# Optimization experiments

Hardware: AMD Instinct MI355X
Metric: run time of the kernel (lower is better)

## Reference

```python
import jax, jax.numpy as jnp
import numpy as np

NUM_HEADS = 8

def _proj(x, w, b):
    # 1x1x1 Conv3d == pointwise linear over channel dim
    return jnp.einsum('bcxyz,oc->boxyz', x, w) + b[None, :, None, None, None]


def setup_inputs() -> dict:
    key = jax.random.key(0)
    ks = jax.random.split(key, 9)
    B, C, X, Y, Z = 2, 256, 48, 48, 48
    s = 0.05
    return {
        'x':  jax.random.normal(ks[0], (B, C, X, Y, Z), dtype=jnp.float32),
        'wq': jax.random.normal(ks[1], (C, C), dtype=jnp.float32) * s,
        'bq': jax.random.normal(ks[2], (C,), dtype=jnp.float32) * s,
        'wk': jax.random.normal(ks[3], (C, C), dtype=jnp.float32) * s,
        'bk': jax.random.normal(ks[4], (C,), dtype=jnp.float32) * s,
        'wv': jax.random.normal(ks[5], (C, C), dtype=jnp.float32) * s,
        'bv': jax.random.normal(ks[6], (C,), dtype=jnp.float32) * s,
        'wo': jax.random.normal(ks[7], (C, C), dtype=jnp.float32) * s,
        'bo': jax.random.normal(ks[8], (C,), dtype=jnp.float32) * s,
    }


def reference(x, wq, bq, wk, bk, wv, bv, wo, bo):
    B, C, X, Y, Z = x.shape
    H = NUM_HEADS
    P = C // H  # per-head channels
    q = _proj(x, wq, bq).reshape(B, H, P, X, Y, Z)
    k = _proj(x, wk, bk).reshape(B, H, P, X, Y, Z)
    v = _proj(x, wv, bv).reshape(B, H, P, X, Y, Z)
    # torch einsum 'bnxyzc,bmxyzc->bnmxy' contracts z and per-head channel c
    scores = jnp.einsum('bncxyz,bmcxyz->bnmxy', q, k) / jnp.sqrt(jnp.float32(P))
    # torch F.softmax(dim=-1) on [b,n,m,x,y] -> softmax over y axis (faithful)
    attn = jax.nn.softmax(scores, axis=-1)
    # torch 'bnmxy,bmxyzc->bnxyzc', then permute/reshape back to [B,C,X,Y,Z]
    out = jnp.einsum('bnmxy,bmcxyz->bncxyz', attn, v).reshape(B, C, X, Y, Z)
    return _proj(out, wo, bo)
```

## Files before the change

kernel.cpp:

```cpp
#include <hip/hip_runtime.h>
#include <hip/hip_bf16.h>
#include <stdint.h>


#define S_TOT 110592
#define NBX   2304

typedef unsigned short u16;
typedef __attribute__((ext_vector_type(8))) short bf16x8;
typedef __attribute__((ext_vector_type(4))) float f32x4;
typedef __attribute__((ext_vector_type(4))) uint32_t u32x4;

__device__ __forceinline__ u16 f2b(float f){
  union { float f; uint32_t u; } v; v.f = f;
  uint32_t u = v.u;
  return (u16)((u + 0x7fffu + ((u >> 16) & 1u)) >> 16);
}
__device__ __forceinline__ float b2f(u16 h){
  union { float f; uint32_t u; } v; v.u = ((uint32_t)h) << 16; return v.f;
}
__device__ __forceinline__ f32x4 mfma16(bf16x8 a, bf16x8 b, f32x4 c){
  return __builtin_amdgcn_mfma_f32_16x16x32_bf16(a, b, c, 0, 0, 0);
}

__global__ __launch_bounds__(256) void k_prep(
    const float* __restrict__ wq, const float* __restrict__ wk,
    const float* __restrict__ wv, const float* __restrict__ wo,
    u16* __restrict__ img)
{
  int idx = blockIdx.x * 256 + threadIdx.x;
  if (idx < 131072){
    int ck = idx >> 14, rem = idx & 16383;
    int r = rem >> 5, i = rem & 31;
    int c = ck * 32 + i;
    float v = (r < 256) ? wq[r * 256 + c] : wk[(r - 256) * 256 + c];
    img[idx] = f2b(v);
  } else if (idx < 196608){
    int l = idx - 131072;
    int ck = l >> 13, rem = l & 8191;
    int r = rem >> 5, i = rem & 31;
    img[idx] = f2b(wv[r * 256 + ck * 32 + i]);
  } else if (idx < 262144){
    int l = idx - 196608;
    int ck = l >> 13, rem = l & 8191;
    int r = rem >> 5, i = rem & 31;
    img[idx] = f2b(wo[r * 256 + ck * 32 + i]);
  }
}

#define K1_LDS 57344
__global__ __launch_bounds__(1024, 4) void k_qk_scores(
    const float* __restrict__ x, const u16* __restrict__ wimg,
    const float* __restrict__ bq, const float* __restrict__ bk,
    float* __restrict__ scores, u16* __restrict__ xws)
{
  extern __shared__ char lds[];
  u16* xT  = (u16*)lds;
  u16* qkz = (u16*)lds;
  float* ps0 = (float*)(lds + 49152);
  float* ps1 = (float*)(lds + 53248);

  const int tid  = threadIdx.x;
  const int wave = tid >> 6, lane = tid & 63;
  const int l15 = lane & 15, l4 = lane >> 4;
  const int bx = blockIdx.x, b = blockIdx.y;
  const int s0 = bx * 96;
  const float* xb = x + (size_t)b * 256 * S_TOT;

  #pragma unroll
  for (int it = 0; it < 3; it++){
    int e = it * 1024 + tid;
    int z = e % 96, c16 = e / 96;
    const float* px = xb + (size_t)(c16 * 8) * S_TOT + s0 + z;
    union { u32x4 q; u16 h[8]; } u;
    #pragma unroll
    for (int i = 0; i < 8; i++) u.h[i] = f2b(px[(size_t)i * S_TOT]);
    *(u32x4*)((char*)xT + z * 512 + ((c16 ^ (z & 7)) << 4)) = u.q;
  }
  __syncthreads();

  if (xws){
    u32x4* vt = (u32x4*)(xws + (size_t)(b * 1152 + bx) * 24576);
    #pragma unroll
    for (int it = 0; it < 3; it++){
      u32x4 q = ((const u32x4*)xT)[it * 1024 + tid];
      __builtin_nontemporal_store(q, vt + it * 1024 + tid);
    }
  }

  const int proj = wave >> 3;
  const int rb = (wave & 7) * 32;
  const float* bias = proj ? bk : bq;

  f32x4 acc[2][6];
  #pragma unroll
  for (int fr = 0; fr < 2; fr++){
    f32x4 iv;
    #pragma unroll
    for (int j = 0; j < 4; j++) iv[j] = bias[rb + fr * 16 + l4 * 4 + j];
    #pragma unroll
    for (int fc = 0; fc < 6; fc++) acc[fr][fc] = iv;
  }
  #pragma unroll
  for (int ck = 0; ck < 8; ck++){
    bf16x8 af[2], bfr[6];
    #pragma unroll
    for (int fr = 0; fr < 2; fr++){
      int row = wave * 32 + fr * 16 + l15;
      af[fr] = *(const bf16x8*)(wimg + ck * 16384 + row * 32 + l4 * 8);
    }
    #pragma unroll
    for (int fc = 0; fc < 6; fc++){
      int z = fc * 16 + l15;
      bfr[fc] = *(const bf16x8*)((char*)xT + z * 512 + (((ck * 4 + l4) ^ (l15 & 7)) << 4));
    }
    #pragma unroll
    for (int fr = 0; fr < 2; fr++)
      #pragma unroll
      for (int fc = 0; fc < 6; fc++)
        acc[fr][fc] = mfma16(af[fr], bfr[fc], acc[fr][fc]);
  }
  __syncthreads();

  const int och = proj * 256 + rb + l4 * 4;
  const int ca = l15 * 32 + l4 * 8;
  const int cb = 256 + (l15 & 7) * 32 + l4 * 8;

  #pragma unroll
  for (int fr = 0; fr < 2; fr++){
    int oc = och + fr * 16;
    #pragma unroll
    for (int fc = 0; fc < 3; fc++){
      int zl = fc * 16 + l15;
      ushort4 u;
      u.x = f2b(acc[fr][fc][0]); u.y = f2b(acc[fr][fc][1]);
      u.z = f2b(acc[fr][fc][2]); u.w = f2b(acc[fr][fc][3]);
      *(ushort4*)((char*)qkz + zl * 1024 + ((((oc >> 3) ^ zl) & 63) << 4)
                  + (oc & 7) * 2) = u;
    }
  }
  __syncthreads();
  {
    f32x4 sc = {0.f, 0.f, 0.f, 0.f};
    #pragma unroll
    for (int zi = 0; zi < 3; zi++){
      int zl = wave * 3 + zi;
      bf16x8 aq  = *(const bf16x8*)((char*)qkz + zl * 1024 + ((((ca >> 3) ^ zl) & 63) << 4));
      bf16x8 bk8 = *(const bf16x8*)((char*)qkz + zl * 1024 + ((((cb >> 3) ^ zl) & 63) << 4));
      sc = mfma16(aq, bk8, sc);
    }
    if (l4 < 2 && l15 < 8){
      #pragma unroll
      for (int j = 0; j < 4; j++)
        ps0[wave * 64 + (l4 * 4 + j) * 8 + l15] = sc[j];
    }
  }
  __syncthreads();

  if (tid < 64){
    float s = 0.f;
    #pragma unroll
    for (int w = 0; w < 16; w++) s += ps0[w * 64 + tid];
    scores[(size_t)(b * 64 + tid) * NBX + bx * 2] = s * 0.17677669529663687f;
  }
  #pragma unroll
  for (int fr = 0; fr < 2; fr++){
    int oc = och + fr * 16;
    #pragma unroll
    for (int fc = 3; fc < 6; fc++){
      int zl = (fc - 3) * 16 + l15;
      ushort4 u;
      u.x = f2b(acc[fr][fc][0]); u.y = f2b(acc[fr][fc][1]);
      u.z = f2b(acc[fr][fc][2]); u.w = f2b(acc[fr][fc][3]);
      *(ushort4*)((char*)qkz + zl * 1024 + ((((oc >> 3) ^ zl) & 63) << 4)
                  + (oc & 7) * 2) = u;
    }
  }
  __syncthreads();
  {
    f32x4 sc = {0.f, 0.f, 0.f, 0.f};
    #pragma unroll
    for (int zi = 0; zi < 3; zi++){
      int zl = wave * 3 + zi;
      bf16x8 aq  = *(const bf16x8*)((char*)qkz + zl * 1024 + ((((ca >> 3) ^ zl) & 63) << 4));
      bf16x8 bk8 = *(const bf16x8*)((char*)qkz + zl * 1024 + ((((cb >> 3) ^ zl) & 63) << 4));
      sc = mfma16(aq, bk8, sc);
    }
    if (l4 < 2 && l15 < 8){
      #pragma unroll
      for (int j = 0; j < 4; j++)
        ps1[wave * 64 + (l4 * 4 + j) * 8 + l15] = sc[j];
    }
  }
  __syncthreads();
  if (tid < 64){
    float s = 0.f;
    #pragma unroll
    for (int w = 0; w < 16; w++) s += ps1[w * 64 + tid];
    scores[(size_t)(b * 64 + tid) * NBX + bx * 2 + 1] = s * 0.17677669529663687f;
  }
}

__global__ __launch_bounds__(256) void k_softmax(
    const float* __restrict__ scores, float* __restrict__ attn)
{
  int row  = blockIdx.x * 4 + (threadIdx.x >> 6);
  int lane = threadIdx.x & 63;
  const float* src = scores + (size_t)row * 48;
  float v = (lane < 48) ? src[lane] : -1e30f;
  float m = v;
  #pragma unroll
  for (int off = 32; off; off >>= 1) m = fmaxf(m, __shfl_xor(m, off));
  float e = (lane < 48) ? __expf(v - m) : 0.f;
  float s = e;
  #pragma unroll
  for (int off = 32; off; off >>= 1) s += __shfl_xor(s, off);
  if (lane < 48) attn[(size_t)row * 48 + lane] = e / s;
}

#define K3_LDS 49664
__global__ __launch_bounds__(512, 4) void k_out_x(
    const u16* __restrict__ xws, const u16* __restrict__ wvimg,
    const u16* __restrict__ woimg, const float* __restrict__ bv,
    const float* __restrict__ bo, const float* __restrict__ attn,
    float* __restrict__ out)
{
  extern __shared__ char lds[];
  u16* xT = (u16*)lds;
  u16* vl = (u16*)lds;
  u16* oT = (u16*)lds;
  float* atl = (float*)(lds + 49152);

  const int tid  = threadIdx.x;
  const int wave = tid >> 6, lane = tid & 63;
  const int l15 = lane & 15, l4 = lane >> 4;
  const int bx = blockIdx.x, b = blockIdx.y;
  const int s0 = bx * 96;

  if (tid < 128)
    atl[tid] = attn[(size_t)(b * 64 + (tid & 63)) * NBX + bx * 2 + (tid >> 6)];

  {
    const u32x4* vt = (const u32x4*)(xws + (size_t)(b * 1152 + bx) * 24576);
    #pragma unroll
    for (int it = 0; it < 6; it++)
      ((u32x4*)xT)[it * 512 + tid] = __builtin_nontemporal_load(&vt[it * 512 + tid]);
  }
  __syncthreads();

  f32x4 vac[2][6];
  #pragma unroll
  for (int fr = 0; fr < 2; fr++){
    f32x4 iv;
    #pragma unroll
    for (int j = 0; j < 4; j++) iv[j] = bv[wave * 32 + fr * 16 + l4 * 4 + j];
    #pragma unroll
    for (int fc = 0; fc < 6; fc++) vac[fr][fc] = iv;
  }
  #pragma unroll
  for (int ck = 0; ck < 8; ck++){
    bf16x8 af[2], bfr[6];
    #pragma unroll
    for (int fr = 0; fr < 2; fr++){
      int row = wave * 32 + fr * 16 + l15;
      af[fr] = *(const bf16x8*)(wvimg + ck * 8192 + row * 32 + l4 * 8);
    }
    #pragma unroll
    for (int fc = 0; fc < 6; fc++){
      int z = fc * 16 + l15;
      bfr[fc] = *(const bf16x8*)((char*)xT + z * 512 + (((ck * 4 + l4) ^ (l15 & 7)) << 4));
    }
    #pragma unroll
    for (int fr = 0; fr < 2; fr++)
      #pragma unroll
      for (int fc = 0; fc < 6; fc++)
        vac[fr][fc] = mfma16(af[fr], bfr[fc], vac[fr][fc]);
  }
  __syncthreads();

  #pragma unroll
  for (int fr = 0; fr < 2; fr++){
    int o0 = wave * 32 + fr * 16 + l4 * 4;
    #pragma unroll
    for (int fc = 0; fc < 6; fc++){
      int z = fc * 16 + l15;
      ushort4 u;
      u.x = f2b(vac[fr][fc][0]); u.y = f2b(vac[fr][fc][1]);
      u.z = f2b(vac[fr][fc][2]); u.w = f2b(vac[fr][fc][3]);
      *(ushort4*)((char*)vl + z * 512 + (((o0 >> 3) ^ (z & 7)) << 4) + (o0 & 7) * 2) = u;
    }
  }
  __syncthreads();

  #pragma unroll
  for (int it = 0; it < 6; it++){
    int e = it * 512 + tid;
    int c16 = e & 31, z = e >> 5;
    int r = c16 & 3, hn = c16 >> 2;
    const float* at = atl + ((z >= 48) ? 64 : 0);
    float a[8] = {0,0,0,0,0,0,0,0};
    #pragma unroll
    for (int m = 0; m < 8; m++){
      union { uint4 q; u16 h[8]; } v8;
      v8.q = *(const uint4*)((char*)vl + z * 512 + (((m * 4 + r) ^ (z & 7)) << 4));
      float am = at[hn * 8 + m];
      #pragma unroll
      for (int i = 0; i < 8; i++) a[i] = fmaf(am, b2f(v8.h[i]), a[i]);
    }
    union { uint4 q; u16 h[8]; } pk;
    #pragma unroll
    for (int i = 0; i < 8; i++) pk.h[i] = f2b(a[i]);
    __syncthreads();
    *(uint4*)((char*)oT + z * 512 + ((c16 ^ (z & 7)) << 4)) = pk.q;
  }
  __syncthreads();

  f32x4 oac[2][6];
  #pragma unroll
  for (int fr = 0; fr < 2; fr++){
    f32x4 iv;
    #pragma unroll
    for (int j = 0; j < 4; j++) iv[j] = bo[wave * 32 + fr * 16 + l4 * 4 + j];
    #pragma unroll
    for (int fc = 0; fc < 6; fc++) oac[fr][fc] = iv;
  }
  #pragma unroll
  for (int ck = 0; ck < 8; ck++){
    bf16x8 af[2], bfr[6];
    #pragma unroll
    for (int fr = 0; fr < 2; fr++){
      int row = wave * 32 + fr * 16 + l15;
      af[fr] = *(const bf16x8*)(woimg + ck * 8192 + row * 32 + l4 * 8);
    }
    #pragma unroll
    for (int fc = 0; fc < 6; fc++){
      int z = fc * 16 + l15;
      bfr[fc] = *(const bf16x8*)((char*)oT + z * 512 + (((ck * 4 + l4) ^ (l15 & 7)) << 4));
    }
    #pragma unroll
    for (int fr = 0; fr < 2; fr++)
      #pragma unroll
      for (int fc = 0; fc < 6; fc++)
        oac[fr][fc] = mfma16(af[fr], bfr[fc], oac[fr][fc]);
  }

  #pragma unroll
  for (int fr = 0; fr < 2; fr++)
    #pragma unroll
    for (int fc = 0; fc < 6; fc++)
      #pragma unroll
      for (int j = 0; j < 4; j++){
        int o = wave * 32 + fr * 16 + l4 * 4 + j;
        int z = fc * 16 + l15;
        __builtin_nontemporal_store(oac[fr][fc][j],
            &out[(size_t)(b * 256 + o) * S_TOT + s0 + z]);
      }
}

__global__ __launch_bounds__(512, 4) void k_out(
    const float* __restrict__ x, const u16* __restrict__ wvimg,
    const u16* __restrict__ woimg, const float* __restrict__ bv,
    const float* __restrict__ bo, const float* __restrict__ attn,
    float* __restrict__ out)
{
  extern __shared__ char lds[];
  u16* xT = (u16*)lds;
  u16* vl = (u16*)lds;
  u16* oT = (u16*)lds;
  float* atl = (float*)(lds + 49152);

  const int tid  = threadIdx.x;
  const int wave = tid >> 6, lane = tid & 63;
  const int l15 = lane & 15, l4 = lane >> 4;
  const int bx = blockIdx.x, b = blockIdx.y;
  const int s0 = bx * 96;
  const float* xb = x + (size_t)b * 256 * S_TOT;

  if (tid < 128)
    atl[tid] = attn[(size_t)(b * 64 + (tid & 63)) * NBX + bx * 2 + (tid >> 6)];

  #pragma unroll
  for (int it = 0; it < 6; it++){
    int e = it * 512 + tid;
    int z = e % 96, c16 = e / 96;
    const float* px = xb + (size_t)(c16 * 8) * S_TOT + s0 + z;
    union { uint4 q; u16 h[8]; } u;
    #pragma unroll
    for (int i = 0; i < 8; i++) u.h[i] = f2b(px[(size_t)i * S_TOT]);
    *(uint4*)((char*)xT + z * 512 + ((c16 ^ (z & 7)) << 4)) = u.q;
  }
  __syncthreads();

  f32x4 vac[2][6];
  #pragma unroll
  for (int fr = 0; fr < 2; fr++){
    f32x4 iv;
    #pragma unroll
    for (int j = 0; j < 4; j++) iv[j] = bv[wave * 32 + fr * 16 + l4 * 4 + j];
    #pragma unroll
    for (int fc = 0; fc < 6; fc++) vac[fr][fc] = iv;
  }
  #pragma unroll
  for (int ck = 0; ck < 8; ck++){
    bf16x8 af[2], bfr[6];
    #pragma unroll
    for (int fr = 0; fr < 2; fr++){
      int row = wave * 32 + fr * 16 + l15;
      af[fr] = *(const bf16x8*)(wvimg + ck * 8192 + row * 32 + l4 * 8);
    }
    #pragma unroll
    for (int fc = 0; fc < 6; fc++){
      int z = fc * 16 + l15;
      bfr[fc] = *(const bf16x8*)((char*)xT + z * 512 + (((ck * 4 + l4) ^ (l15 & 7)) << 4));
    }
    #pragma unroll
    for (int fr = 0; fr < 2; fr++)
      #pragma unroll
      for (int fc = 0; fc < 6; fc++)
        vac[fr][fc] = mfma16(af[fr], bfr[fc], vac[fr][fc]);
  }
  __syncthreads();

  #pragma unroll
  for (int fr = 0; fr < 2; fr++){
    int o0 = wave * 32 + fr * 16 + l4 * 4;
    #pragma unroll
    for (int fc = 0; fc < 6; fc++){
      int z = fc * 16 + l15;
      ushort4 u;
      u.x = f2b(vac[fr][fc][0]); u.y = f2b(vac[fr][fc][1]);
      u.z = f2b(vac[fr][fc][2]); u.w = f2b(vac[fr][fc][3]);
      *(ushort4*)((char*)vl + z * 512 + (((o0 >> 3) ^ (z & 7)) << 4) + (o0 & 7) * 2) = u;
    }
  }
  __syncthreads();

  #pragma unroll
  for (int it = 0; it < 6; it++){
    int e = it * 512 + tid;
    int c16 = e & 31, z = e >> 5;
    int r = c16 & 3, hn = c16 >> 2;
    const float* at = atl + ((z >= 48) ? 64 : 0);
    float a[8] = {0,0,0,0,0,0,0,0};
    #pragma unroll
    for (int m = 0; m < 8; m++){
      union { uint4 q; u16 h[8]; } v8;
      v8.q = *(const uint4*)((char*)vl + z * 512 + (((m * 4 + r) ^ (z & 7)) << 4));
      float am = at[hn * 8 + m];
      #pragma unroll
      for (int i = 0; i < 8; i++) a[i] = fmaf(am, b2f(v8.h[i]), a[i]);
    }
    union { uint4 q; u16 h[8]; } pk;
    #pragma unroll
    for (int i = 0; i < 8; i++) pk.h[i] = f2b(a[i]);
    __syncthreads();
    *(uint4*)((char*)oT + z * 512 + ((c16 ^ (z & 7)) << 4)) = pk.q;
  }
  __syncthreads();

  f32x4 oac[2][6];
  #pragma unroll
  for (int fr = 0; fr < 2; fr++){
    f32x4 iv;
    #pragma unroll
    for (int j = 0; j < 4; j++) iv[j] = bo[wave * 32 + fr * 16 + l4 * 4 + j];
    #pragma unroll
    for (int fc = 0; fc < 6; fc++) oac[fr][fc] = iv;
  }
  #pragma unroll
  for (int ck = 0; ck < 8; ck++){
    bf16x8 af[2], bfr[6];
    #pragma unroll
    for (int fr = 0; fr < 2; fr++){
      int row = wave * 32 + fr * 16 + l15;
      af[fr] = *(const bf16x8*)(woimg + ck * 8192 + row * 32 + l4 * 8);
    }
    #pragma unroll
    for (int fc = 0; fc < 6; fc++){
      int z = fc * 16 + l15;
      bfr[fc] = *(const bf16x8*)((char*)oT + z * 512 + (((ck * 4 + l4) ^ (l15 & 7)) << 4));
    }
    #pragma unroll
    for (int fr = 0; fr < 2; fr++)
      #pragma unroll
      for (int fc = 0; fc < 6; fc++)
        oac[fr][fc] = mfma16(af[fr], bfr[fc], oac[fr][fc]);
  }

  #pragma unroll
  for (int fr = 0; fr < 2; fr++)
    #pragma unroll
    for (int fc = 0; fc < 6; fc++)
      #pragma unroll
      for (int j = 0; j < 4; j++){
        int o = wave * 32 + fr * 16 + l4 * 4 + j;
        int z = fc * 16 + l15;
        __builtin_nontemporal_store(oac[fr][fc][j],
            &out[(size_t)(b * 256 + o) * S_TOT + s0 + z]);
      }
}

extern "C" void kernel_launch(void* const* d_in, const int* in_sizes, int n_in,
                              void* d_out, int out_size, void* d_ws, size_t ws_size,
                              hipStream_t stream) {
  (void)in_sizes; (void)n_in; (void)out_size;
  const float* x  = (const float*)d_in[0];
  const float* wq = (const float*)d_in[1];
  const float* bq = (const float*)d_in[2];
  const float* wk = (const float*)d_in[3];
  const float* bk = (const float*)d_in[4];
  const float* wv = (const float*)d_in[5];
  const float* bv = (const float*)d_in[6];
  const float* wo = (const float*)d_in[7];
  const float* bo = (const float*)d_in[8];
  float* out = (float*)d_out;

  char* ws = (char*)d_ws;
  u16*  wimg   = (u16*)ws;
  u16*  wvimg  = wimg + 131072;
  u16*  woimg  = wimg + 196608;
  float* scores = (float*)(ws + 524288);
  float* attn   = (float*)(ws + 1703936);
  u16*  xws     = (u16*)(ws + 2883584);

  const size_t need = 2883584 + 113246208;
  const bool fused = (ws_size >= need);

  k_prep<<<1024, 256, 0, stream>>>(wq, wk, wv, wo, wimg);
  k_qk_scores<<<dim3(1152, 2), 1024, K1_LDS, stream>>>(
      x, wimg, bq, bk, scores, fused ? xws : (u16*)nullptr);
  k_softmax<<<1536, 256, 0, stream>>>(scores, attn);
  if (fused){
    k_out_x<<<dim3(1152, 2), 512, K3_LDS, stream>>>(
        xws, wvimg, woimg, bv, bo, attn, out);
  } else {
    k_out<<<dim3(1152, 2), 512, K3_LDS, stream>>>(
        x, wvimg, woimg, bv, bo, attn, out);
  }
}
```

Measured before the change: 227.1 us.

## Add dedicated transpose kernel converting x to bf16 channel-chunked layout

Adds a separate k_tr kernel that reads x with coalesced 16-byte loads, transposes through LDS, and writes a bf16 buffer laid out as [b][channel-chunk of 32][spatial][32]. Both the QK-scores kernel and the output kernel then stage their tiles from this buffer instead of k_qk_scores doing strided scalar fp32 loads and writing the per-tile copy. The aim is to replace uncoalesced per-channel reads of x with a bandwidth-friendly transpose. In exchange it adds a kernel launch and an extra full write and read of the bf16 copy. The old path is kept as a fallback kernel for when the workspace is too small.

After: 250.0 us. 1.1x slower.

```diff
diff --git a/kernel.cpp b/kernel.cpp
--- a/kernel.cpp
+++ b/kernel.cpp
@@ -48,11 +48,61 @@
   }
 }
 
+#define TR_LDS 52224
+__global__ __launch_bounds__(256) void k_tr(
+    const float* __restrict__ x, u16* __restrict__ xws)
+{
+  extern __shared__ u16 T[];
+  const int tid = threadIdx.x;
+  const int bc = blockIdx.y;
+  const int b = bc >> 3, ck = bc & 7;
+  const size_t xbase = ((size_t)(b * 256 + ck * 32)) * S_TOT + (size_t)blockIdx.x * 768;
+
+  #pragma unroll
+  for (int i = 0; i < 24; i++){
+    int idx = i * 256 + tid;
+    int c = idx / 192, f4 = idx % 192;
+    const u32x4* p = (const u32x4*)(x + xbase + (size_t)c * S_TOT + f4 * 4);
+    union { u32x4 v; float f[4]; } uu;
+    uu.v = __builtin_nontemporal_load(p);
+    #pragma unroll
+    for (int j = 0; j < 4; j++)
+      T[(f4 * 4 + j) * 34 + c] = f2b(uu.f[j]);
+  }
+  __syncthreads();
+
+  u16* dst = xws + (size_t)bc * S_TOT * 32 + (size_t)blockIdx.x * 768 * 32;
+  #pragma unroll
+  for (int i = 0; i < 12; i++){
+    int g4 = i * 256 + tid;
+    int s = g4 >> 2, pq = g4 & 3;
+    union { u32x4 v; u16 h[8]; } o;
+    #pragma unroll
+    for (int j = 0; j < 8; j++) o.h[j] = T[s * 34 + pq * 8 + j];
+    *(u32x4*)(dst + (size_t)g4 * 8) = o.v;
+  }
+}
+
+template<int NTHR>
+__device__ __forceinline__ void stage_from_xws(
+    const u16* srcb, int s0, int tid, u16* xT)
+{
+  #pragma unroll
+  for (int it = 0; it < 3072 / NTHR; it++){
+    int g = it * NTHR + tid;
+    int ck = g / 384, r = g % 384;
+    int s = r >> 2, cq = r & 3;
+    u32x4 q = *(const u32x4*)(srcb + ((size_t)ck * S_TOT + s0 + s) * 32 + cq * 8);
+    int c16 = ck * 4 + cq;
+    *(u32x4*)((char*)xT + s * 512 + ((c16 ^ (s & 7)) << 4)) = q;
+  }
+}
+
 #define K1_LDS 57344
 __global__ __launch_bounds__(1024, 4) void k_qk_scores(
-    const float* __restrict__ x, const u16* __restrict__ wimg,
+    const u16* __restrict__ xws, const u16* __restrict__ wimg,
     const float* __restrict__ bq, const float* __restrict__ bk,
-    float* __restrict__ scores, u16* __restrict__ xws)
+    float* __restrict__ scores)
 {
   extern __shared__ char lds[];
   u16* xT  = (u16*)lds;
@@ -65,28 +115,9 @@
   const int l15 = lane & 15, l4 = lane >> 4;
   const int bx = blockIdx.x, b = blockIdx.y;
   const int s0 = bx * 96;
-  const float* xb = x + (size_t)b * 256 * S_TOT;
-
-  #pragma unroll
-  for (int it = 0; it < 3; it++){
-    int e = it * 1024 + tid;
-    int z = e % 96, c16 = e / 96;
-    const float* px = xb + (size_t)(c16 * 8) * S_TOT + s0 + z;
-    union { u32x4 q; u16 h[8]; } u;
-    #pragma unroll
-    for (int i = 0; i < 8; i++) u.h[i] = f2b(px[(size_t)i * S_TOT]);
-    *(u32x4*)((char*)xT + z * 512 + ((c16 ^ (z & 7)) << 4)) = u.q;
-  }
-  __syncthreads();
-
-  if (xws){
-    u32x4* vt = (u32x4*)(xws + (size_t)(b * 1152 + bx) * 24576);
-    #pragma unroll
-    for (int it = 0; it < 3; it++){
-      u32x4 q = ((const u32x4*)xT)[it * 1024 + tid];
-      __builtin_nontemporal_store(q, vt + it * 1024 + tid);
-    }
-  }
+
+  stage_from_xws<1024>(xws + (size_t)b * 8 * S_TOT * 32, s0, tid, xT);
+  __syncthreads();
 
   const int proj = wave >> 3;
   const int rb = (wave & 7) * 32;
@@ -156,7 +187,6 @@
     }
   }
   __syncthreads();
-
   if (tid < 64){
     float s = 0.f;
     #pragma unroll
@@ -201,6 +231,148 @@
   }
 }
 
+__global__ __launch_bounds__(1024, 4) void k_qk_fb(
+    const float* __restrict__ x, const u16* __restrict__ wimg,
+    const float* __restrict__ bq, const float* __restrict__ bk,
+    float* __restrict__ scores)
+{
+  extern __shared__ char lds[];
+  u16* xT  = (u16*)lds;
+  u16* qkz = (u16*)lds;
+  float* ps0 = (float*)(lds + 49152);
+  float* ps1 = (float*)(lds + 53248);
+
+  const int tid  = threadIdx.x;
+  const int wave = tid >> 6, lane = tid & 63;
+  const int l15 = lane & 15, l4 = lane >> 4;
+  const int bx = blockIdx.x, b = blockIdx.y;
+  const int s0 = bx * 96;
+  const float* xb = x + (size_t)b * 256 * S_TOT;
+
+  #pragma unroll
+  for (int it = 0; it < 3; it++){
+    int e = it * 1024 + tid;
+    int z = e % 96, c16 = e / 96;
+    const float* px = xb + (size_t)(c16 * 8) * S_TOT + s0 + z;
+    union { u32x4 q; u16 h[8]; } u;
+    #pragma unroll
+    for (int i = 0; i < 8; i++) u.h[i] = f2b(px[(size_t)i * S_TOT]);
+    *(u32x4*)((char*)xT + z * 512 + ((c16 ^ (z & 7)) << 4)) = u.q;
+  }
+  __syncthreads();
+
+  const int proj = wave >> 3;
+  const int rb = (wave & 7) * 32;
+  const float* bias = proj ? bk : bq;
+
+  f32x4 acc[2][6];
+  #pragma unroll
+  for (int fr = 0; fr < 2; fr++){
+    f32x4 iv;
+    #pragma unroll
+    for (int j = 0; j < 4; j++) iv[j] = bias[rb + fr * 16 + l4 * 4 + j];
+    #pragma unroll
+    for (int fc = 0; fc < 6; fc++) acc[fr][fc] = iv;
+  }
+  #pragma unroll
+  for (int ck = 0; ck < 8; ck++){
+    bf16x8 af[2], bfr[6];
+    #pragma unroll
+    for (int fr = 0; fr < 2; fr++){
+      int row = wave * 32 + fr * 16 + l15;
+      af[fr] = *(const bf16x8*)(wimg + ck * 16384 + row * 32 + l4 * 8);
+    }
+    #pragma unroll
+    for (int fc = 0; fc < 6; fc++){
+      int z = fc * 16 + l15;
+      bfr[fc] = *(const bf16x8*)((char*)xT + z * 512 + (((ck * 4 + l4) ^ (l15 & 7)) << 4));
+    }
+    #pragma unroll
+    for (int fr = 0; fr < 2; fr++)
+      #pragma unroll
+      for (int fc = 0; fc < 6; fc++)
+        acc[fr][fc] = mfma16(af[fr], bfr[fc], acc[fr][fc]);
+  }
+  __syncthreads();
+
+  const int och = proj * 256 + rb + l4 * 4;
+  const int ca = l15 * 32 + l4 * 8;
+  const int cb = 256 + (l15 & 7) * 32 + l4 * 8;
+
+  #pragma unroll
+  for (int fr = 0; fr < 2; fr++){
+    int oc = och + fr * 16;
+    #pragma unroll
+    for (int fc = 0; fc < 3; fc++){
+      int zl = fc * 16 + l15;
+      ushort4 u;
+      u.x = f2b(acc[fr][fc][0]); u.y = f2b(acc[fr][fc][1]);
+      u.z = f2b(acc[fr][fc][2]); u.w = f2b(acc[fr][fc][3]);
+      *(ushort4*)((char*)qkz + zl * 1024 + ((((oc >> 3) ^ zl) & 63) << 4)
+                  + (oc & 7) * 2) = u;
+    }
+  }
+  __syncthreads();
+  {
+    f32x4 sc = {0.f, 0.f, 0.f, 0.f};
+    #pragma unroll
+    for (int zi = 0; zi < 3; zi++){
+      int zl = wave * 3 + zi;
+      bf16x8 aq  = *(const bf16x8*)((char*)qkz + zl * 1024 + ((((ca >> 3) ^ zl) & 63) << 4));
+      bf16x8 bk8 = *(const bf16x8*)((char*)qkz + zl * 1024 + ((((cb >> 3) ^ zl) & 63) << 4));
+      sc = mfma16(aq, bk8, sc);
+    }
+    if (l4 < 2 && l15 < 8){
+      #pragma unroll
+      for (int j = 0; j < 4; j++)
+        ps0[wave * 64 + (l4 * 4 + j) * 8 + l15] = sc[j];
+    }
+  }
+  __syncthreads();
+  if (tid < 64){
+    float s = 0.f;
+    #pragma unroll
+    for (int w = 0; w < 16; w++) s += ps0[w * 64 + tid];
+    scores[(size_t)(b * 64 + tid) * NBX + bx * 2] = s * 0.17677669529663687f;
+  }
+  #pragma unroll
+  for (int fr = 0; fr < 2; fr++){
+    int oc = och + fr * 16;
+    #pragma unroll
+    for (int fc = 3; fc < 6; fc++){
+      int zl = (fc - 3) * 16 + l15;
+      ushort4 u;
+      u.x = f2b(acc[fr][fc][0]); u.y = f2b(acc[fr][fc][1]);
+      u.z = f2b(acc[fr][fc][2]); u.w = f2b(acc[fr][fc][3]);
+      *(ushort4*)((char*)qkz + zl * 1024 + ((((oc >> 3) ^ zl) & 63) << 4)
+                  + (oc & 7) * 2) = u;
+    }
+  }
+  __syncthreads();
+  {
+    f32x4 sc = {0.f, 0.f, 0.f, 0.f};
+    #pragma unroll
+    for (int zi = 0; zi < 3; zi++){
+      int zl = wave * 3 + zi;
+      bf16x8 aq  = *(const bf16x8*)((char*)qkz + zl * 1024 + ((((ca >> 3) ^ zl) & 63) << 4));
+      bf16x8 bk8 = *(const bf16x8*)((char*)qkz + zl * 1024 + ((((cb >> 3) ^ zl) & 63) << 4));
+      sc = mfma16(aq, bk8, sc);
+    }
+    if (l4 < 2 && l15 < 8){
+      #pragma unroll
+      for (int j = 0; j < 4; j++)
+        ps1[wave * 64 + (l4 * 4 + j) * 8 + l15] = sc[j];
+    }
+  }
+  __syncthreads();
+  if (tid < 64){
+    float s = 0.f;
+    #pragma unroll
+    for (int w = 0; w < 16; w++) s += ps1[w * 64 + tid];
+    scores[(size_t)(b * 64 + tid) * NBX + bx * 2 + 1] = s * 0.17677669529663687f;
+  }
+}
+
 __global__ __launch_bounds__(256) void k_softmax(
     const float* __restrict__ scores, float* __restrict__ attn)
 {
@@ -216,6 +388,126 @@
   #pragma unroll
   for (int off = 32; off; off >>= 1) s += __shfl_xor(s, off);
   if (lane < 48) attn[(size_t)row * 48 + lane] = e / s;
+}
+
+__device__ __forceinline__ void k3_body(
+    char* lds, int tid, int wave, int lane, int l15, int l4,
+    int bx, int b, const u16* wvimg, const u16* woimg,
+    const float* bv, const float* bo, float* out)
+{
+  u16* xT = (u16*)lds;
+  u16* vl = (u16*)lds;
+  u16* oT = (u16*)lds;
+  float* atl = (float*)(lds + 49152);
+  const int s0 = bx * 96;
+
+  f32x4 vac[2][6];
+  #pragma unroll
+  for (int fr = 0; fr < 2; fr++){
+    f32x4 iv;
+    #pragma unroll
+    for (int j = 0; j < 4; j++) iv[j] = bv[wave * 32 + fr * 16 + l4 * 4 + j];
+    #pragma unroll
+    for (int fc = 0; fc < 6; fc++) vac[fr][fc] = iv;
+  }
+  #pragma unroll
+  for (int ck = 0; ck < 8; ck++){
+    bf16x8 af[2], bfr[6];
+    #pragma unroll
+    for (int fr = 0; fr < 2; fr++){
+      int row = wave * 32 + fr * 16 + l15;
+      af[fr] = *(const bf16x8*)(wvimg + ck * 8192 + row * 32 + l4 * 8);
+    }
+    #pragma unroll
+    for (int fc = 0; fc < 6; fc++){
+      int z = fc * 16 + l15;
+      bfr[fc] = *(const bf16x8*)((char*)xT + z * 512 + (((ck * 4 + l4) ^ (l15 & 7)) << 4));
+    }
+    #pragma unroll
+    for (int fr = 0; fr < 2; fr++)
+      #pragma unroll
+      for (int fc = 0; fc < 6; fc++)
+        vac[fr][fc] = mfma16(af[fr], bfr[fc], vac[fr][fc]);
+  }
+  __syncthreads();
+
+  #pragma unroll
+  for (int fr = 0; fr < 2; fr++){
+    int o0 = wave * 32 + fr * 16 + l4 * 4;
+    #pragma unroll
+    for (int fc = 0; fc < 6; fc++){
+      int z = fc * 16 + l15;
+      ushort4 u;
+      u.x = f2b(vac[fr][fc][0]); u.y = f2b(vac[fr][fc][1]);
+      u.z = f2b(vac[fr][fc][2]); u.w = f2b(vac[fr][fc][3]);
+      *(ushort4*)((char*)vl + z * 512 + (((o0 >> 3) ^ (z & 7)) << 4) + (o0 & 7) * 2) = u;
+    }
+  }
+  __syncthreads();
+
+  #pragma unroll
+  for (int it = 0; it < 6; it++){
+    int e = it * 512 + tid;
+    int c16 = e & 31, z = e >> 5;
+    int r = c16 & 3, hn = c16 >> 2;
+    const float* at = atl + ((z >= 48) ? 64 : 0);
+    float a[8] = {0,0,0,0,0,0,0,0};
+    #pragma unroll
+    for (int m = 0; m < 8; m++){
+      union { uint4 q; u16 h[8]; } v8;
+      v8.q = *(const uint4*)((char*)vl + z * 512 + (((m * 4 + r) ^ (z & 7)) << 4));
+      float am = at[hn * 8 + m];
+      #pragma unroll
+      for (int i = 0; i < 8; i++) a[i] = fmaf(am, b2f(v8.h[i]), a[i]);
+    }
+    union { uint4 q; u16 h[8]; } pk;
+    #pragma unroll
+    for (int i = 0; i < 8; i++) pk.h[i] = f2b(a[i]);
+    __syncthreads();
+    *(uint4*)((char*)oT + z * 512 + ((c16 ^ (z & 7)) << 4)) = pk.q;
+  }
+  __syncthreads();
+
+  f32x4 oac[2][6];
+  #pragma unroll
+  for (int fr = 0; fr < 2; fr++){
+    f32x4 iv;
+    #pragma unroll
+    for (int j = 0; j < 4; j++) iv[j] = bo[wave * 32 + fr * 16 + l4 * 4 + j];
+    #pragma unroll
+    for (int fc = 0; fc < 6; fc++) oac[fr][fc] = iv;
+  }
+  #pragma unroll
+  for (int ck = 0; ck < 8; ck++){
+    bf16x8 af[2], bfr[6];
+    #pragma unroll
+    for (int fr = 0; fr < 2; fr++){
+      int row = wave * 32 + fr * 16 + l15;
+      af[fr] = *(const bf16x8*)(woimg + ck * 8192 + row * 32 + l4 * 8);
+    }
+    #pragma unroll
+    for (int fc = 0; fc < 6; fc++){
+      int z = fc * 16 + l15;
+      bfr[fc] = *(const bf16x8*)((char*)oT + z * 512 + (((ck * 4 + l4) ^ (l15 & 7)) << 4));
+    }
+    #pragma unroll
+    for (int fr = 0; fr < 2; fr++)
+      #pragma unroll
+      for (int fc = 0; fc < 6; fc++)
+        oac[fr][fc] = mfma16(af[fr], bfr[fc], oac[fr][fc]);
+  }
+
+  #pragma unroll
+  for (int fr = 0; fr < 2; fr++)
+    #pragma unroll
+    for (int fc = 0; fc < 6; fc++)
+      #pragma unroll
+      for (int j = 0; j < 4; j++){
+        int o = wave * 32 + fr * 16 + l4 * 4 + j;
+        int z = fc * 16 + l15;
+        __builtin_nontemporal_store(oac[fr][fc][j],
+            &out[(size_t)(b * 256 + o) * S_TOT + s0 + z]);
+      }
 }
 
 #define K3_LDS 49664
@@ -226,135 +518,19 @@
     float* __restrict__ out)
 {
   extern __shared__ char lds[];
-  u16* xT = (u16*)lds;
-  u16* vl = (u16*)lds;
-  u16* oT = (u16*)lds;
   float* atl = (float*)(lds + 49152);
-
   const int tid  = threadIdx.x;
   const int wave = tid >> 6, lane = tid & 63;
   const int l15 = lane & 15, l4 = lane >> 4;
   const int bx = blockIdx.x, b = blockIdx.y;
-  const int s0 = bx * 96;
 
   if (tid < 128)
     atl[tid] = attn[(size_t)(b * 64 + (tid & 63)) * NBX + bx * 2 + (tid >> 6)];
 
-  {
-    const u32x4* vt = (const u32x4*)(xws + (size_t)(b * 1152 + bx) * 24576);
-    #pragma unroll
-    for (int it = 0; it < 6; it++)
-      ((u32x4*)xT)[it * 512 + tid] = __builtin_nontemporal_load(&vt[it * 512 + tid]);
-  }
-  __syncthreads();
-
-  f32x4 vac[2][6];
-  #pragma unroll
-  for (int fr = 0; fr < 2; fr++){
-    f32x4 iv;
-    #pragma unroll
-    for (int j = 0; j < 4; j++) iv[j] = bv[wave * 32 + fr * 16 + l4 * 4 + j];
-    #pragma unroll
-    for (int fc = 0; fc < 6; fc++) vac[fr][fc] = iv;
-  }
-  #pragma unroll
-  for (int ck = 0; ck < 8; ck++){
-    bf16x8 af[2], bfr[6];
-    #pragma unroll
-    for (int fr = 0; fr < 2; fr++){
-      int row = wave * 32 + fr * 16 + l15;
-      af[fr] = *(const bf16x8*)(wvimg + ck * 8192 + row * 32 + l4 * 8);
-    }
-    #pragma unroll
-    for (int fc = 0; fc < 6; fc++){
-      int z = fc * 16 + l15;
-      bfr[fc] = *(const bf16x8*)((char*)xT + z * 512 + (((ck * 4 + l4) ^ (l15 & 7)) << 4));
-    }
-    #pragma unroll
-    for (int fr = 0; fr < 2; fr++)
-      #pragma unroll
-      for (int fc = 0; fc < 6; fc++)
-        vac[fr][fc] = mfma16(af[fr], bfr[fc], vac[fr][fc]);
-  }
-  __syncthreads();
-
-  #pragma unroll
-  for (int fr = 0; fr < 2; fr++){
-    int o0 = wave * 32 + fr * 16 + l4 * 4;
-    #pragma unroll
-    for (int fc = 0; fc < 6; fc++){
-      int z = fc * 16 + l15;
-      ushort4 u;
-      u.x = f2b(vac[fr][fc][0]); u.y = f2b(vac[fr][fc][1]);
-      u.z = f2b(vac[fr][fc][2]); u.w = f2b(vac[fr][fc][3]);
-      *(ushort4*)((char*)vl + z * 512 + (((o0 >> 3) ^ (z & 7)) << 4) + (o0 & 7) * 2) = u;
-    }
-  }
-  __syncthreads();
-
-  #pragma unroll
-  for (int it = 0; it < 6; it++){
-    int e = it * 512 + tid;
-    int c16 = e & 31, z = e >> 5;
-    int r = c16 & 3, hn = c16 >> 2;
-    const float* at = atl + ((z >= 48) ? 64 : 0);
-    float a[8] = {0,0,0,0,0,0,0,0};
-    #pragma unroll
-    for (int m = 0; m < 8; m++){
-      union { uint4 q; u16 h[8]; } v8;
-      v8.q = *(const uint4*)((char*)vl + z * 512 + (((m * 4 + r) ^ (z & 7)) << 4));
-      float am = at[hn * 8 + m];
-      #pragma unroll
-      for (int i = 0; i < 8; i++) a[i] = fmaf(am, b2f(v8.h[i]), a[i]);
-    }
-    union { uint4 q; u16 h[8]; } pk;
-    #pragma unroll
-    for (int i = 0; i < 8; i++) pk.h[i] = f2b(a[i]);
-    __syncthreads();
-    *(uint4*)((char*)oT + z * 512 + ((c16 ^ (z & 7)) << 4)) = pk.q;
-  }
-  __syncthreads();
-
-  f32x4 oac[2][6];
-  #pragma unroll
-  for (int fr = 0; fr < 2; fr++){
-    f32x4 iv;
-    #pragma unroll
-    for (int j = 0; j < 4; j++) iv[j] = bo[wave * 32 + fr * 16 + l4 * 4 + j];
-    #pragma unroll
-    for (int fc = 0; fc < 6; fc++) oac[fr][fc] = iv;
-  }
-  #pragma unroll
-  for (int ck = 0; ck < 8; ck++){
-    bf16x8 af[2], bfr[6];
-    #pragma unroll
-    for (int fr = 0; fr < 2; fr++){
-      int row = wave * 32 + fr * 16 + l15;
-      af[fr] = *(const bf16x8*)(woimg + ck * 8192 + row * 32 + l4 * 8);
-    }
-    #pragma unroll
-    for (int fc = 0; fc < 6; fc++){
-      int z = fc * 16 + l15;
-      bfr[fc] = *(const bf16x8*)((char*)oT + z * 512 + (((ck * 4 + l4) ^ (l15 & 7)) << 4));
-    }
-    #pragma unroll
-    for (int fr = 0; fr < 2; fr++)
-      #pragma unroll
-      for (int fc = 0; fc < 6; fc++)
-        oac[fr][fc] = mfma16(af[fr], bfr[fc], oac[fr][fc]);
-  }
-
-  #pragma unroll
-  for (int fr = 0; fr < 2; fr++)
-    #pragma unroll
-    for (int fc = 0; fc < 6; fc++)
-      #pragma unroll
-      for (int j = 0; j < 4; j++){
-        int o = wave * 32 + fr * 16 + l4 * 4 + j;
-        int z = fc * 16 + l15;
-        __builtin_nontemporal_store(oac[fr][fc][j],
-            &out[(size_t)(b * 256 + o) * S_TOT + s0 + z]);
-      }
+  stage_from_xws<512>(xws + (size_t)b * 8 * S_TOT * 32, bx * 96, tid, (u16*)lds);
+  __syncthreads();
+
+  k3_body(lds, tid, wave, lane, l15, l4, bx, b, wvimg, woimg, bv, bo, out);
 }
 
 __global__ __launch_bounds__(512, 4) void k_out(
@@ -365,10 +541,7 @@
 {
   extern __shared__ char lds[];
   u16* xT = (u16*)lds;
-  u16* vl = (u16*)lds;
-  u16* oT = (u16*)lds;
   float* atl = (float*)(lds + 49152);
-
   const int tid  = threadIdx.x;
   const int wave = tid >> 6, lane = tid & 63;
   const int l15 = lane & 15, l4 = lane >> 4;
@@ -384,120 +557,14 @@
     int e = it * 512 + tid;
     int z = e % 96, c16 = e / 96;
     const float* px = xb + (size_t)(c16 * 8) * S_TOT + s0 + z;
-    union { uint4 q; u16 h[8]; } u;
+    union { u32x4 q; u16 h[8]; } u;
     #pragma unroll
     for (int i = 0; i < 8; i++) u.h[i] = f2b(px[(size_t)i * S_TOT]);
-    *(uint4*)((char*)xT + z * 512 + ((c16 ^ (z & 7)) << 4)) = u.q;
-  }
-  __syncthreads();
-
-  f32x4 vac[2][6];
-  #pragma unroll
-  for (int fr = 0; fr < 2; fr++){
-    f32x4 iv;
-    #pragma unroll
-    for (int j = 0; j < 4; j++) iv[j] = bv[wave * 32 + fr * 16 + l4 * 4 + j];
-    #pragma unroll
-    for (int fc = 0; fc < 6; fc++) vac[fr][fc] = iv;
-  }
-  #pragma unroll
-  for (int ck = 0; ck < 8; ck++){
-    bf16x8 af[2], bfr[6];
-    #pragma unroll
-    for (int fr = 0; fr < 2; fr++){
-      int row = wave * 32 + fr * 16 + l15;
-      af[fr] = *(const bf16x8*)(wvimg + ck * 8192 + row * 32 + l4 * 8);
-    }
-    #pragma unroll
-    for (int fc = 0; fc < 6; fc++){
-      int z = fc * 16 + l15;
-      bfr[fc] = *(const bf16x8*)((char*)xT + z * 512 + (((ck * 4 + l4) ^ (l15 & 7)) << 4));
-    }
-    #pragma unroll
-    for (int fr = 0; fr < 2; fr++)
-      #pragma unroll
-      for (int fc = 0; fc < 6; fc++)
-        vac[fr][fc] = mfma16(af[fr], bfr[fc], vac[fr][fc]);
-  }
-  __syncthreads();
-
-  #pragma unroll
-  for (int fr = 0; fr < 2; fr++){
-    int o0 = wave * 32 + fr * 16 + l4 * 4;
-    #pragma unroll
-    for (int fc = 0; fc < 6; fc++){
-      int z = fc * 16 + l15;
-      ushort4 u;
-      u.x = f2b(vac[fr][fc][0]); u.y = f2b(vac[fr][fc][1]);
-      u.z = f2b(vac[fr][fc][2]); u.w = f2b(vac[fr][fc][3]);
-      *(ushort4*)((char*)vl + z * 512 + (((o0 >> 3) ^ (z & 7)) << 4) + (o0 & 7) * 2) = u;
-    }
-  }
-  __syncthreads();
-
-  #pragma unroll
-  for (int it = 0; it < 6; it++){
-    int e = it * 512 + tid;
-    int c16 = e & 31, z = e >> 5;
-    int r = c16 & 3, hn = c16 >> 2;
-    const float* at = atl + ((z >= 48) ? 64 : 0);
-    float a[8] = {0,0,0,0,0,0,0,0};
-    #pragma unroll
-    for (int m = 0; m < 8; m++){
-      union { uint4 q; u16 h[8]; } v8;
-      v8.q = *(const uint4*)((char*)vl + z * 512 + (((m * 4 + r) ^ (z & 7)) << 4));
-      float am = at[hn * 8 + m];
-      #pragma unroll
-      for (int i = 0; i < 8; i++) a[i] = fmaf(am, b2f(v8.h[i]), a[i]);
-    }
-    union { uint4 q; u16 h[8]; } pk;
-    #pragma unroll
-    for (int i = 0; i < 8; i++) pk.h[i] = f2b(a[i]);
-    __syncthreads();
-    *(uint4*)((char*)oT + z * 512 + ((c16 ^ (z & 7)) << 4)) = pk.q;
-  }
-  __syncthreads();
-
-  f32x4 oac[2][6];
-  #pragma unroll
-  for (int fr = 0; fr < 2; fr++){
-    f32x4 iv;
-    #pragma unroll
-    for (int j = 0; j < 4; j++) iv[j] = bo[wave * 32 + fr * 16 + l4 * 4 + j];
-    #pragma unroll
-    for (int fc = 0; fc < 6; fc++) oac[fr][fc] = iv;
-  }
-  #pragma unroll
-  for (int ck = 0; ck < 8; ck++){
-    bf16x8 af[2], bfr[6];
-    #pragma unroll
-    for (int fr = 0; fr < 2; fr++){
-      int row = wave * 32 + fr * 16 + l15;
-      af[fr] = *(const bf16x8*)(woimg + ck * 8192 + row * 32 + l4 * 8);
-    }
-    #pragma unroll
-    for (int fc = 0; fc < 6; fc++){
-      int z = fc * 16 + l15;
-      bfr[fc] = *(const bf16x8*)((char*)oT + z * 512 + (((ck * 4 + l4) ^ (l15 & 7)) << 4));
-    }
-    #pragma unroll
-    for (int fr = 0; fr < 2; fr++)
-      #pragma unroll
-      for (int fc = 0; fc < 6; fc++)
-        oac[fr][fc] = mfma16(af[fr], bfr[fc], oac[fr][fc]);
-  }
-
-  #pragma unroll
-  for (int fr = 0; fr < 2; fr++)
-    #pragma unroll
-    for (int fc = 0; fc < 6; fc++)
-      #pragma unroll
-      for (int j = 0; j < 4; j++){
-        int o = wave * 32 + fr * 16 + l4 * 4 + j;
-        int z = fc * 16 + l15;
-        __builtin_nontemporal_store(oac[fr][fc][j],
-            &out[(size_t)(b * 256 + o) * S_TOT + s0 + z]);
-      }
+    *(u32x4*)((char*)xT + z * 512 + ((c16 ^ (z & 7)) << 4)) = u.q;
+  }
+  __syncthreads();
+
+  k3_body(lds, tid, wave, lane, l15, l4, bx, b, wvimg, woimg, bv, bo, out);
 }
 
 extern "C" void kernel_launch(void* const* d_in, const int* in_sizes, int n_in,
@@ -527,8 +594,12 @@
   const bool fused = (ws_size >= need);
 
   k_prep<<<1024, 256, 0, stream>>>(wq, wk, wv, wo, wimg);
-  k_qk_scores<<<dim3(1152, 2), 1024, K1_LDS, stream>>>(
-      x, wimg, bq, bk, scores, fused ? xws : (u16*)nullptr);
+  if (fused){
+    k_tr<<<dim3(144, 16), 256, TR_LDS, stream>>>(x, xws);
+    k_qk_scores<<<dim3(1152, 2), 1024, K1_LDS, stream>>>(xws, wimg, bq, bk, scores);
+  } else {
+    k_qk_fb<<<dim3(1152, 2), 1024, K1_LDS, stream>>>(x, wimg, bq, bk, scores);
+  }
   k_softmax<<<1536, 256, 0, stream>>>(scores, attn);
   if (fused){
     k_out_x<<<dim3(1152, 2), 512, K3_LDS, stream>>>(
```
